# Kernel tuning notes

Hardware: AMD Instinct MI355X
Metric: run time of the kernel (lower is better)

## Reference

```python
import jax, jax.numpy as jnp
import numpy as np

B, T, E = 4, 1024, 1024
H, MULT = 16, 2
HD = E // H
SCALE = HD ** -0.5


def setup_inputs() -> dict:
    key = jax.random.key(0)
    ks = jax.random.split(key, 9)
    s = 0.02
    return {
        "hidden_states": jax.random.normal(ks[0], (B, T, E), jnp.float32),
        "attention_mask": jnp.zeros((B, 1, T, T), jnp.float32),
        "Wq": jax.random.normal(ks[1], (E, E), jnp.float32) * s,
        "bq": jnp.zeros((E,), jnp.float32),
        "Wk": jax.random.normal(ks[2], (MULT * E, E), jnp.float32) * s,
        "bk": jnp.zeros((MULT * E,), jnp.float32),
        "Wv": jax.random.normal(ks[3], (MULT * E, E), jnp.float32) * s,
        "bv": jnp.zeros((MULT * E,), jnp.float32),
        "Wo": jax.random.normal(ks[4], (E, E), jnp.float32) * s,
        "bo": jnp.zeros((E,), jnp.float32),
    }


def reference(hidden_states, attention_mask, Wq, bq, Wk, bk, Wv, bv, Wo, bo):
    x = hidden_states  # [B, T, E]
    # q projection, scaled
    q = (jnp.einsum("bte,fe->btf", x, Wq) + bq) * SCALE  # [B,T,E]
    q = q.reshape(B, T, H, HD).transpose(0, 2, 1, 3)      # [B,H,T,HD]
    # k/v project to multiplier-expanded dim, then _shape with seq_len=-1:
    # [B,T,MULT*E] -> view(B, T*MULT, H, HD) (torch view semantics) -> [B,H,T*MULT,HD]
    k = jnp.einsum("bte,fe->btf", x, Wk) + bk             # [B,T,MULT*E]
    k = k.reshape(B, T * MULT, H, HD).transpose(0, 2, 1, 3)
    v = jnp.einsum("bte,fe->btf", x, Wv) + bv
    v = v.reshape(B, T * MULT, H, HD).transpose(0, 2, 1, 3)

    S = T * MULT  # src_len; src_len0 = T
    attn = jnp.einsum("bhtd,bhsd->bhts", q, k)            # [B,H,T,S]
    # custom mask broadcast: view src as [MULT, src_len0] and add mask[:, :, :, None, :]
    attn = attn.reshape(B, H, T, MULT, T) + attention_mask[:, :, :, None, :]
    attn = attn.reshape(B, H, T, S)
    attn = jax.nn.softmax(attn, axis=-1)
    out = jnp.einsum("bhts,bhsd->bhtd", attn, v)          # [B,H,T,HD]
    out = out.transpose(0, 2, 1, 3).reshape(B, T, E)
    out = jnp.einsum("bte,fe->btf", out, Wo) + bo
    return out
```

## Files before the change

kernel.cpp:

```cpp
#include <hip/hip_runtime.h>
#include <math.h>

#define BB    4
#define TT    1024
#define EE    1024
#define HH    16
#define HDIM  64
#define SS    2048
#define MROWS 4096
#define QSCALE 0.18033688011112f
#define LOG2E  1.4426950408889634f

typedef short  s8v  __attribute__((ext_vector_type(8)));
typedef float  f4v  __attribute__((ext_vector_type(4)));

__device__ __forceinline__ unsigned short f2bf(float f) {
    union { float f; unsigned u; } c; c.f = f;
    unsigned u = c.u + 0x7FFFu + ((c.u >> 16) & 1u);
    return (unsigned short)(u >> 16);
}
__device__ __forceinline__ float bflo(unsigned u) {
    union { unsigned u; float f; } c; c.u = u << 16; return c.f;
}
__device__ __forceinline__ float bfhi(unsigned u) {
    union { unsigned u; float f; } c; c.u = u & 0xffff0000u; return c.f;
}

__device__ __forceinline__ void async16(const void* g, void* l) {
    __builtin_amdgcn_global_load_lds(
        (const __attribute__((address_space(1))) unsigned int*)g,
        (__attribute__((address_space(3))) unsigned int*)l,
        16, 0, 0);
}

__global__ __launch_bounds__(256) void cvt6_kernel(
    const float* __restrict__ x,  const float* __restrict__ wq,
    const float* __restrict__ wk, const float* __restrict__ wv,
    const float* __restrict__ wo, const float* __restrict__ mk,
    unsigned short* __restrict__ xb,  unsigned short* __restrict__ wqb,
    unsigned short* __restrict__ wkb, unsigned short* __restrict__ wvb,
    unsigned short* __restrict__ wob, unsigned short* __restrict__ mbb)
{
    const int total = 3670016;
    int i = blockIdx.x * 256 + threadIdx.x;
    const int stride = gridDim.x * 256;
    for (; i < total; i += stride) {
        const float* s; unsigned short* d; int off; float sc = 1.0f;
        if (i < 1048576)      { s = x;  d = xb;  off = i; }
        else if (i < 1310720) { s = wq; d = wqb; off = i - 1048576; }
        else if (i < 1835008) { s = wk; d = wkb; off = i - 1310720; }
        else if (i < 2359296) { s = wv; d = wvb; off = i - 1835008; }
        else if (i < 2621440) { s = wo; d = wob; off = i - 2359296; }
        else                  { s = mk; d = mbb; off = i - 2621440; sc = LOG2E; }
        float4 v = ((const float4*)s)[off];
        ushort4 o;
        o.x = f2bf(v.x * sc); o.y = f2bf(v.y * sc);
        o.z = f2bf(v.z * sc); o.w = f2bf(v.w * sc);
        ((ushort4*)d)[off] = o;
    }
}

#define GEMM_KLOOP(Aptr, Wptr, Ksz)                                            \
    for (int k0 = 0; k0 < (Ksz); k0 += 32) {                                   \
        _Pragma("unroll")                                                      \
        for (int it = 0; it < 2; ++it) {                                       \
            int f = (it * 4 + w) * 64 + lane;                                  \
            int r = f >> 2, g = (f & 3) * 8;                                   \
            async16((Aptr) + (size_t)(m0 + r) * (Ksz) + k0 + g,                \
                    As + (it * 4 + w) * 512);                                  \
            async16((Wptr) + (size_t)(n0 + r) * (Ksz) + k0 + g,                \
                    Bs + (it * 4 + w) * 512);                                  \
        }                                                                      \
        __syncthreads();                                                       \
        s8v af[4], bf[4];                                                      \
        _Pragma("unroll")                                                      \
        for (int i = 0; i < 4; ++i)                                            \
            af[i] = *(const s8v*)(As + (wm + i * 16 + col16) * 32 + quad * 8); \
        _Pragma("unroll")                                                      \
        for (int j = 0; j < 4; ++j)                                            \
            bf[j] = *(const s8v*)(Bs + (wn + j * 16 + col16) * 32 + quad * 8); \
        _Pragma("unroll")                                                      \
        for (int i = 0; i < 4; ++i)                                            \
            _Pragma("unroll")                                                  \
            for (int j = 0; j < 4; ++j)                                        \
                acc[i][j] = __builtin_amdgcn_mfma_f32_16x16x32_bf16(           \
                    af[i], bf[j], acc[i][j], 0, 0, 0);                         \
        __syncthreads();                                                       \
    }

__global__ __launch_bounds__(256, 3) void gemm_qk_kernel(
    const unsigned short* __restrict__ X,  const unsigned short* __restrict__ Wq,
    const unsigned short* __restrict__ Wk, const float* __restrict__ bq,
    const float* __restrict__ bk, unsigned short* __restrict__ qp,
    unsigned short* __restrict__ kp)
{
    __shared__ __align__(16) unsigned short As[128 * 32];
    __shared__ __align__(16) unsigned short Bs[128 * 32];

    const int tid = threadIdx.x;
    const int lane = tid & 63, w = tid >> 6;
    const int wm = (w & 1) * 64, wn = (w >> 1) * 64;
    const int col16 = lane & 15, quad = lane >> 4;
    const int m0 = blockIdx.x * 128;
    const bool isQ = blockIdx.y < 8;
    const int n0 = blockIdx.y * 128;
    const unsigned short* Wrow = isQ ? Wq + (size_t)n0 * EE
                                     : Wk + (size_t)(n0 - EE) * EE;

    f4v acc[4][4];
#pragma unroll
    for (int i = 0; i < 4; ++i)
#pragma unroll
        for (int j = 0; j < 4; ++j) acc[i][j] = (f4v)0.0f;

    for (int k0 = 0; k0 < EE; k0 += 32) {
#pragma unroll
        for (int it = 0; it < 2; ++it) {
            int f = (it * 4 + w) * 64 + lane;
            int r = f >> 2, g = (f & 3) * 8;
            async16(X + (size_t)(m0 + r) * EE + k0 + g, As + (it * 4 + w) * 512);
            async16(Wrow + (size_t)r * EE + k0 + g, Bs + (it * 4 + w) * 512);
        }
        __syncthreads();
        s8v af[4], bf[4];
#pragma unroll
        for (int i = 0; i < 4; ++i)
            af[i] = *(const s8v*)(As + (wm + i * 16 + col16) * 32 + quad * 8);
#pragma unroll
        for (int j = 0; j < 4; ++j)
            bf[j] = *(const s8v*)(Bs + (wn + j * 16 + col16) * 32 + quad * 8);
#pragma unroll
        for (int i = 0; i < 4; ++i)
#pragma unroll
            for (int j = 0; j < 4; ++j)
                acc[i][j] = __builtin_amdgcn_mfma_f32_16x16x32_bf16(
                    af[i], bf[j], acc[i][j], 0, 0, 0);
        __syncthreads();
    }

#pragma unroll
    for (int j = 0; j < 4; ++j) {
        const int n = n0 + wn + j * 16 + col16;
        const float bn = isQ ? bq[n] : bk[n - EE];
#pragma unroll
        for (int i = 0; i < 4; ++i) {
            const int mb = m0 + wm + i * 16 + quad * 4;
#pragma unroll
            for (int r = 0; r < 4; ++r) {
                const int m = mb + r;
                float c = acc[i][j][r] + bn;
                if (isQ) {
                    qp[(size_t)m * EE + n] = f2bf(c * QSCALE);
                } else {
                    const int nk = n - EE;
                    const int mm = nk >> 10, h = (nk >> 6) & 15, d = nk & 63;
                    const int b_ = m >> 10, t = m & 1023;
                    const int s = 2 * t + mm;
                    kp[((size_t)(b_ * HH + h) * SS + s) * HDIM + d] = f2bf(c);
                }
            }
        }
    }
}

template <int LAYOUT, int OUTF32, int Ksz, int Nsz>
__global__ __launch_bounds__(256, 3) void gemm_mfma_kernel(
    const unsigned short* __restrict__ A, const unsigned short* __restrict__ W,
    const float* __restrict__ bias, void* __restrict__ Cout, float alpha)
{
    __shared__ __align__(16) unsigned short As[128 * 32];
    __shared__ __align__(16) unsigned short Bs[128 * 32];

    const int tid = threadIdx.x;
    const int lane = tid & 63, w = tid >> 6;
    const int wm = (w & 1) * 64, wn = (w >> 1) * 64;
    const int col16 = lane & 15, quad = lane >> 4;
    const int m0 = blockIdx.x * 128;
    const int n0 = blockIdx.y * 128;

    f4v acc[4][4];
#pragma unroll
    for (int i = 0; i < 4; ++i)
#pragma unroll
        for (int j = 0; j < 4; ++j) acc[i][j] = (f4v)0.0f;

    GEMM_KLOOP(A, W, Ksz)

#pragma unroll
    for (int j = 0; j < 4; ++j) {
        const int n = n0 + wn + j * 16 + col16;
        const float bn = (LAYOUT == 2) ? 0.0f : bias[n];
#pragma unroll
        for (int i = 0; i < 4; ++i) {
            const int mb = m0 + wm + i * 16 + quad * 4;
#pragma unroll
            for (int r = 0; r < 4; ++r) {
                const int m = mb + r;
                float c = (acc[i][j][r] + ((LAYOUT == 2) ? bias[m] : bn)) * alpha;
                if (LAYOUT == 0) {
                    if (OUTF32) ((float*)Cout)[(size_t)m * Nsz + n] = c;
                    else ((unsigned short*)Cout)[(size_t)m * Nsz + n] = f2bf(c);
                } else {
                    const int mm = m >> 10, h = (m >> 6) & 15, d = m & 63;
                    const int b_ = n >> 10, t = n & 1023;
                    const int s = 2 * t + mm;
                    ((unsigned short*)Cout)[((size_t)(b_ * HH + h) * HDIM + d) * SS + s] = f2bf(c);
                }
            }
        }
    }
}

__global__ __launch_bounds__(256, 4) void attn_mfma3_kernel(
    const unsigned short* __restrict__ Q, const unsigned short* __restrict__ Kh,
    const unsigned short* __restrict__ Vt, const unsigned short* __restrict__ Mb,
    unsigned short* __restrict__ O)
{
    constexpr int PT = 68;
    __shared__ __align__(16) unsigned short K0[64 * PT];
    __shared__ __align__(16) unsigned short K1[64 * PT];
    __shared__ __align__(16) unsigned short V0[64 * PT];
    __shared__ __align__(16) unsigned short V1[64 * PT];

    const int tid = threadIdx.x;
    const int lane = tid & 63, w = tid >> 6;
    const int col16 = lane & 15, quad = lane >> 4;

    const int gid = blockIdx.x;
    const int v = gid & 7, j = gid >> 3;
    const int bh = v * 8 + (j >> 4);
    const int t0 = (j & 15) * 64;
    const int b_ = bh >> 4, h = bh & 15;

    const unsigned short* Qrow =
        Q + (size_t)(b_ * TT + t0 + w * 16 + col16) * EE + h * HDIM;
    const s8v qf0 = *(const s8v*)(Qrow + quad * 8);
    const s8v qf1 = *(const s8v*)(Qrow + 32 + quad * 8);

    f4v oacc[4];
#pragma unroll
    for (int jd = 0; jd < 4; ++jd) oacc[jd] = (f4v)0.0f;
    float mrun = -INFINITY;
    f4v l4 = (f4v)0.0f;

    const unsigned short* Kb   = Kh + (size_t)bh * SS * HDIM;
    const unsigned short* Vb   = Vt + (size_t)bh * HDIM * SS;
    const unsigned short* Mrow = Mb + (size_t)b_ * TT * TT
                               + (size_t)(t0 + w * 16 + col16) * TT;
    const int myrow = (w * 16 + col16) * PT;

    for (int it16 = 0; it16 < 16; ++it16) {
        const int t2b = it16 * 64;

        uint2 mm[4];
#pragma unroll
        for (int js = 0; js < 4; ++js)
            mm[js] = *(const uint2*)(Mrow + t2b + js * 16 + quad * 4);

        __syncthreads();
#pragma unroll
        for (int st = 0; st < 2; ++st) {
            int idx = tid + st * 256;
            int r = idx >> 3, c = (idx & 7) * 8;
            *(uint4*)(K0 + r * PT + c) = *(const uint4*)(Kb + (size_t)(t2b + r) * HDIM + c);
            *(uint4*)(K1 + r * PT + c) = *(const uint4*)(Kb + (size_t)(1024 + t2b + r) * HDIM + c);
            *(uint4*)(V0 + r * PT + c) = *(const uint4*)(Vb + (size_t)r * SS + t2b + c);
            *(uint4*)(V1 + r * PT + c) = *(const uint4*)(Vb + (size_t)r * SS + 1024 + t2b + c);
        }
        __syncthreads();

        f4v s0acc[4], s1acc[4];
#pragma unroll
        for (int js = 0; js < 4; ++js) {
            f4v mv;
            mv[0] = bflo(mm[js].x); mv[1] = bfhi(mm[js].x);
            mv[2] = bflo(mm[js].y); mv[3] = bfhi(mm[js].y);
            s0acc[js] = mv; s1acc[js] = mv;
        }
#pragma unroll
        for (int ks = 0; ks < 2; ++ks) {
            const s8v bq_ = ks ? qf1 : qf0;
#pragma unroll
            for (int js = 0; js < 4; ++js) {
                s8v ak0 = *(const s8v*)(K0 + (js * 16 + col16) * PT + ks * 32 + quad * 8);
                s8v ak1 = *(const s8v*)(K1 + (js * 16 + col16) * PT + ks * 32 + quad * 8);
                s0acc[js] = __builtin_amdgcn_mfma_f32_16x16x32_bf16(ak0, bq_, s0acc[js], 0, 0, 0);
                s1acc[js] = __builtin_amdgcn_mfma_f32_16x16x32_bf16(ak1, bq_, s1acc[js], 0, 0, 0);
            }
        }

        float tm0 = fmaxf(fmaxf(s0acc[0][0], s0acc[0][1]), fmaxf(s0acc[0][2], s0acc[0][3]));
        float tm1 = fmaxf(fmaxf(s0acc[1][0], s0acc[1][1]), fmaxf(s0acc[1][2], s0acc[1][3]));
        float tm2 = fmaxf(fmaxf(s0acc[2][0], s0acc[2][1]), fmaxf(s0acc[2][2], s0acc[2][3]));
        float tm3 = fmaxf(fmaxf(s0acc[3][0], s0acc[3][1]), fmaxf(s0acc[3][2], s0acc[3][3]));
        float tn0 = fmaxf(fmaxf(s1acc[0][0], s1acc[0][1]), fmaxf(s1acc[0][2], s1acc[0][3]));
        float tn1 = fmaxf(fmaxf(s1acc[1][0], s1acc[1][1]), fmaxf(s1acc[1][2], s1acc[1][3]));
        float tn2 = fmaxf(fmaxf(s1acc[2][0], s1acc[2][1]), fmaxf(s1acc[2][2], s1acc[2][3]));
        float tn3 = fmaxf(fmaxf(s1acc[3][0], s1acc[3][1]), fmaxf(s1acc[3][2], s1acc[3][3]));
        float tmax = fmaxf(fmaxf(fmaxf(tm0, tm1), fmaxf(tm2, tm3)),
                           fmaxf(fmaxf(tn0, tn1), fmaxf(tn2, tn3)));

        if (!__all(tmax - mrun <= 10.0f)) {
            float tfull = fmaxf(tmax, __shfl_xor(tmax, 16));
            tfull = fmaxf(tfull, __shfl_xor(tfull, 32));
            const float mnew = fmaxf(mrun, tfull);
            const float scl = __builtin_amdgcn_exp2f(mrun - mnew);
            l4 *= scl;
            float sclr[4];
#pragma unroll
            for (int r = 0; r < 4; ++r) sclr[r] = __shfl(scl, quad * 4 + r);
#pragma unroll
            for (int jd = 0; jd < 4; ++jd)
#pragma unroll
                for (int r = 0; r < 4; ++r) oacc[jd][r] *= sclr[r];
            mrun = mnew;
        }

        unsigned pk0[8], pk1[8];
#pragma unroll
        for (int js = 0; js < 4; ++js) {
            f4v p0 = s0acc[js] - mrun;
            f4v p1 = s1acc[js] - mrun;
#pragma unroll
            for (int r = 0; r < 4; ++r) {
                p0[r] = __builtin_amdgcn_exp2f(p0[r]);
                p1[r] = __builtin_amdgcn_exp2f(p1[r]);
            }
            l4 += p0 + p1;
            __asm__("v_cvt_pk_bf16_f32 %0, %1, %2" : "=v"(pk0[js*2])   : "v"(p0[0]), "v"(p0[1]));
            __asm__("v_cvt_pk_bf16_f32 %0, %1, %2" : "=v"(pk0[js*2+1]) : "v"(p0[2]), "v"(p0[3]));
            __asm__("v_cvt_pk_bf16_f32 %0, %1, %2" : "=v"(pk1[js*2])   : "v"(p1[0]), "v"(p1[1]));
            __asm__("v_cvt_pk_bf16_f32 %0, %1, %2" : "=v"(pk1[js*2+1]) : "v"(p1[2]), "v"(p1[3]));
        }

        __syncthreads();

#pragma unroll
        for (int js = 0; js < 4; ++js) {
            *(uint2*)(K0 + myrow + js * 16 + quad * 4) = make_uint2(pk0[js*2], pk0[js*2+1]);
            *(uint2*)(K1 + myrow + js * 16 + quad * 4) = make_uint2(pk1[js*2], pk1[js*2+1]);
        }
        __syncthreads();

#pragma unroll
        for (int ks = 0; ks < 2; ++ks) {
            s8v p0 = *(const s8v*)(K0 + myrow + ks * 32 + quad * 8);
            s8v p1 = *(const s8v*)(K1 + myrow + ks * 32 + quad * 8);
#pragma unroll
            for (int jd = 0; jd < 4; ++jd) {
                s8v v0_ = *(const s8v*)(V0 + (jd * 16 + col16) * PT + ks * 32 + quad * 8);
                s8v v1_ = *(const s8v*)(V1 + (jd * 16 + col16) * PT + ks * 32 + quad * 8);
                oacc[jd] = __builtin_amdgcn_mfma_f32_16x16x32_bf16(p0, v0_, oacc[jd], 0, 0, 0);
                oacc[jd] = __builtin_amdgcn_mfma_f32_16x16x32_bf16(p1, v1_, oacc[jd], 0, 0, 0);
            }
        }
    }

    float lr = l4[0] + l4[1] + l4[2] + l4[3];
    lr += __shfl_xor(lr, 16);
    lr += __shfl_xor(lr, 32);
    const float inv = 1.0f / lr;
    float invr[4];
#pragma unroll
    for (int r = 0; r < 4; ++r) invr[r] = __shfl(inv, quad * 4 + r);
#pragma unroll
    for (int r = 0; r < 4; ++r) {
        const int t = t0 + w * 16 + quad * 4 + r;
#pragma unroll
        for (int jd = 0; jd < 4; ++jd)
            O[(size_t)(b_ * TT + t) * EE + h * HDIM + jd * 16 + col16] =
                f2bf(oacc[jd][r] * invr[r]);
    }
}

extern "C" void kernel_launch(void* const* d_in, const int* in_sizes, int n_in,
                              void* d_out, int out_size, void* d_ws, size_t ws_size,
                              hipStream_t stream)
{
    (void)in_sizes; (void)n_in; (void)out_size; (void)ws_size;

    const float* x    = (const float*)d_in[0];
    const float* mask = (const float*)d_in[1];
    const float* Wq   = (const float*)d_in[2];
    const float* bq   = (const float*)d_in[3];
    const float* Wk   = (const float*)d_in[4];
    const float* bk   = (const float*)d_in[5];
    const float* Wv   = (const float*)d_in[6];
    const float* bv   = (const float*)d_in[7];
    const float* Wo   = (const float*)d_in[8];
    const float* bo   = (const float*)d_in[9];
    float* out = (float*)d_out;

    unsigned short* xb  = (unsigned short*)d_ws;
    unsigned short* wqb = xb  + (size_t)MROWS * EE;
    unsigned short* wkb = wqb + (size_t)EE * EE;
    unsigned short* wvb = wkb + (size_t)2 * EE * EE;
    unsigned short* wob = wvb + (size_t)2 * EE * EE;
    unsigned short* mb  = wob + (size_t)EE * EE;
    unsigned short* qp  = mb  + (size_t)BB * TT * TT;
    unsigned short* kp  = qp  + (size_t)MROWS * EE;
    unsigned short* vt  = kp  + (size_t)BB * HH * SS * HDIM;
    unsigned short* ao  = vt  + (size_t)BB * HH * SS * HDIM;

    dim3 blk(256);

    cvt6_kernel<<<4096, blk, 0, stream>>>(x, Wq, Wk, Wv, Wo, mask,
                                          xb, wqb, wkb, wvb, wob, mb);
    gemm_qk_kernel<<<dim3(32, 24), blk, 0, stream>>>(xb, wqb, wkb, bq, bk, qp, kp);
    gemm_mfma_kernel<2, 0, EE, MROWS><<<dim3(16, 32), blk, 0, stream>>>(
        wvb, xb, bv, vt, 1.0f);
    attn_mfma3_kernel<<<dim3(1024), blk, 0, stream>>>(qp, kp, vt, mb, ao);
    gemm_mfma_kernel<0, 1, EE, EE><<<dim3(32, 8), blk, 0, stream>>>(
        ao, wob, bo, out, 1.0f);
}
```

Baseline: 268.2 us.

## Prefetch next K/V/mask tile into registers during attention compute

Result: slower. 370.9 us (+38.3%).

```diff
diff --git a/kernel.cpp b/kernel.cpp
--- a/kernel.cpp
+++ b/kernel.cpp
@@ -211,7 +211,7 @@
     }
 }
 
-__global__ __launch_bounds__(256, 4) void attn_mfma3_kernel(
+__global__ __launch_bounds__(256, 4) void attn_mfma4_kernel(
     const unsigned short* __restrict__ Q, const unsigned short* __restrict__ Kh,
     const unsigned short* __restrict__ Vt, const unsigned short* __restrict__ Mb,
     unsigned short* __restrict__ O)
@@ -248,35 +248,57 @@
     const unsigned short* Mrow = Mb + (size_t)b_ * TT * TT
                                + (size_t)(t0 + w * 16 + col16) * TT;
     const int myrow = (w * 16 + col16) * PT;
+    const int r0 = tid >> 3, c0 = (tid & 7) * 8;
+
+    uint4 kv[8];
+    uint2 mmc[4];
+
+#define PREF_KV(T2B)                                                           \
+    kv[0] = *(const uint4*)(Kb + (size_t)((T2B) + r0) * HDIM + c0);            \
+    kv[1] = *(const uint4*)(Kb + (size_t)((T2B) + r0 + 32) * HDIM + c0);       \
+    kv[2] = *(const uint4*)(Kb + (size_t)(1024 + (T2B) + r0) * HDIM + c0);     \
+    kv[3] = *(const uint4*)(Kb + (size_t)(1024 + (T2B) + r0 + 32) * HDIM + c0);\
+    kv[4] = *(const uint4*)(Vb + (size_t)r0 * SS + (T2B) + c0);                \
+    kv[5] = *(const uint4*)(Vb + (size_t)(r0 + 32) * SS + (T2B) + c0);         \
+    kv[6] = *(const uint4*)(Vb + (size_t)r0 * SS + 1024 + (T2B) + c0);         \
+    kv[7] = *(const uint4*)(Vb + (size_t)(r0 + 32) * SS + 1024 + (T2B) + c0);
+
+    PREF_KV(0)
+#pragma unroll
+    for (int js = 0; js < 4; ++js)
+        mmc[js] = *(const uint2*)(Mrow + js * 16 + quad * 4);
 
     for (int it16 = 0; it16 < 16; ++it16) {
-        const int t2b = it16 * 64;
-
-        uint2 mm[4];
-#pragma unroll
-        for (int js = 0; js < 4; ++js)
-            mm[js] = *(const uint2*)(Mrow + t2b + js * 16 + quad * 4);
-
         __syncthreads();
-#pragma unroll
-        for (int st = 0; st < 2; ++st) {
-            int idx = tid + st * 256;
-            int r = idx >> 3, c = (idx & 7) * 8;
-            *(uint4*)(K0 + r * PT + c) = *(const uint4*)(Kb + (size_t)(t2b + r) * HDIM + c);
-            *(uint4*)(K1 + r * PT + c) = *(const uint4*)(Kb + (size_t)(1024 + t2b + r) * HDIM + c);
-            *(uint4*)(V0 + r * PT + c) = *(const uint4*)(Vb + (size_t)r * SS + t2b + c);
-            *(uint4*)(V1 + r * PT + c) = *(const uint4*)(Vb + (size_t)r * SS + 1024 + t2b + c);
-        }
+
+        *(uint4*)(K0 + r0 * PT + c0)        = kv[0];
+        *(uint4*)(K0 + (r0 + 32) * PT + c0) = kv[1];
+        *(uint4*)(K1 + r0 * PT + c0)        = kv[2];
+        *(uint4*)(K1 + (r0 + 32) * PT + c0) = kv[3];
+        *(uint4*)(V0 + r0 * PT + c0)        = kv[4];
+        *(uint4*)(V0 + (r0 + 32) * PT + c0) = kv[5];
+        *(uint4*)(V1 + r0 * PT + c0)        = kv[6];
+        *(uint4*)(V1 + (r0 + 32) * PT + c0) = kv[7];
         __syncthreads();
 
         f4v s0acc[4], s1acc[4];
 #pragma unroll
         for (int js = 0; js < 4; ++js) {
             f4v mv;
-            mv[0] = bflo(mm[js].x); mv[1] = bfhi(mm[js].x);
-            mv[2] = bflo(mm[js].y); mv[3] = bfhi(mm[js].y);
+            mv[0] = bflo(mmc[js].x); mv[1] = bfhi(mmc[js].x);
+            mv[2] = bflo(mmc[js].y); mv[3] = bfhi(mmc[js].y);
             s0acc[js] = mv; s1acc[js] = mv;
         }
+
+        {
+            const int t2n = ((it16 + 1) & 15) * 64;
+            PREF_KV(t2n)
+#pragma unroll
+            for (int js = 0; js < 4; ++js)
+                mmc[js] = *(const uint2*)(Mrow + t2n + js * 16 + quad * 4);
+        }
+
+        __builtin_amdgcn_s_setprio(1);
 #pragma unroll
         for (int ks = 0; ks < 2; ++ks) {
             const s8v bq_ = ks ? qf1 : qf0;
@@ -288,6 +310,7 @@
                 s1acc[js] = __builtin_amdgcn_mfma_f32_16x16x32_bf16(ak1, bq_, s1acc[js], 0, 0, 0);
             }
         }
+        __builtin_amdgcn_s_setprio(0);
 
         float tm0 = fmaxf(fmaxf(s0acc[0][0], s0acc[0][1]), fmaxf(s0acc[0][2], s0acc[0][3]));
         float tm1 = fmaxf(fmaxf(s0acc[1][0], s0acc[1][1]), fmaxf(s0acc[1][2], s0acc[1][3]));
@@ -340,8 +363,8 @@
             *(uint2*)(K0 + myrow + js * 16 + quad * 4) = make_uint2(pk0[js*2], pk0[js*2+1]);
             *(uint2*)(K1 + myrow + js * 16 + quad * 4) = make_uint2(pk1[js*2], pk1[js*2+1]);
         }
-        __syncthreads();
-
+
+        __builtin_amdgcn_s_setprio(1);
 #pragma unroll
         for (int ks = 0; ks < 2; ++ks) {
             s8v p0 = *(const s8v*)(K0 + myrow + ks * 32 + quad * 8);
@@ -354,7 +377,9 @@
                 oacc[jd] = __builtin_amdgcn_mfma_f32_16x16x32_bf16(p1, v1_, oacc[jd], 0, 0, 0);
             }
         }
-    }
+        __builtin_amdgcn_s_setprio(0);
+    }
+#undef PREF_KV
 
     float lr = l4[0] + l4[1] + l4[2] + l4[3];
     lr += __shfl_xor(lr, 16);
@@ -409,7 +434,7 @@
     gemm_qk_kernel<<<dim3(32, 24), blk, 0, stream>>>(xb, wqb, wkb, bq, bk, qp, kp);
     gemm_mfma_kernel<2, 0, EE, MROWS><<<dim3(16, 32), blk, 0, stream>>>(
         wvb, xb, bv, vt, 1.0f);
-    attn_mfma3_kernel<<<dim3(1024), blk, 0, stream>>>(qp, kp, vt, mb, ao);
+    attn_mfma4_kernel<<<dim3(1024), blk, 0, stream>>>(qp, kp, vt, mb, ao);
     gemm_mfma_kernel<0, 1, EE, EE><<<dim3(32, 8), blk, 0, stream>>>(
         ao, wob, bo, out, 1.0f);
 }
```

## Prefetch next K/V/mask tiles into registers and drop a redundant barrier

Applied to the files above, without the earlier changes.

Result: faster. 258.5 us (-3.6%).

```diff
diff --git a/kernel.cpp b/kernel.cpp
--- a/kernel.cpp
+++ b/kernel.cpp
@@ -211,7 +211,7 @@
     }
 }
 
-__global__ __launch_bounds__(256, 4) void attn_mfma3_kernel(
+__global__ __launch_bounds__(256, 4) void attn_mfma5_kernel(
     const unsigned short* __restrict__ Q, const unsigned short* __restrict__ Kh,
     const unsigned short* __restrict__ Vt, const unsigned short* __restrict__ Mb,
     unsigned short* __restrict__ O)
@@ -248,35 +248,68 @@
     const unsigned short* Mrow = Mb + (size_t)b_ * TT * TT
                                + (size_t)(t0 + w * 16 + col16) * TT;
     const int myrow = (w * 16 + col16) * PT;
+    const int r0 = tid >> 3, c0 = (tid & 7) * 8;
+
+    uint4 kA0, kA1, kB0, kB1;
+    uint4 vA0, vA1, vB0, vB1;
+    uint2 mA0, mA1, mA2, mA3;
+
+#define PREF_K(T2B)                                                            \
+    kA0 = *(const uint4*)(Kb + (size_t)((T2B) + r0) * HDIM + c0);              \
+    kA1 = *(const uint4*)(Kb + (size_t)((T2B) + r0 + 32) * HDIM + c0);         \
+    kB0 = *(const uint4*)(Kb + (size_t)(1024 + (T2B) + r0) * HDIM + c0);       \
+    kB1 = *(const uint4*)(Kb + (size_t)(1024 + (T2B) + r0 + 32) * HDIM + c0);
+#define PREF_V(T2B)                                                            \
+    vA0 = *(const uint4*)(Vb + (size_t)r0 * SS + (T2B) + c0);                  \
+    vA1 = *(const uint4*)(Vb + (size_t)(r0 + 32) * SS + (T2B) + c0);           \
+    vB0 = *(const uint4*)(Vb + (size_t)r0 * SS + 1024 + (T2B) + c0);           \
+    vB1 = *(const uint4*)(Vb + (size_t)(r0 + 32) * SS + 1024 + (T2B) + c0);
+#define PREF_M(T2B)                                                            \
+    mA0 = *(const uint2*)(Mrow + (T2B) + 0 * 16 + quad * 4);                   \
+    mA1 = *(const uint2*)(Mrow + (T2B) + 1 * 16 + quad * 4);                   \
+    mA2 = *(const uint2*)(Mrow + (T2B) + 2 * 16 + quad * 4);                   \
+    mA3 = *(const uint2*)(Mrow + (T2B) + 3 * 16 + quad * 4);
+
+    PREF_K(0)
+    PREF_V(0)
+    PREF_M(0)
 
     for (int it16 = 0; it16 < 16; ++it16) {
-        const int t2b = it16 * 64;
-
-        uint2 mm[4];
-#pragma unroll
-        for (int js = 0; js < 4; ++js)
-            mm[js] = *(const uint2*)(Mrow + t2b + js * 16 + quad * 4);
-
         __syncthreads();
-#pragma unroll
-        for (int st = 0; st < 2; ++st) {
-            int idx = tid + st * 256;
-            int r = idx >> 3, c = (idx & 7) * 8;
-            *(uint4*)(K0 + r * PT + c) = *(const uint4*)(Kb + (size_t)(t2b + r) * HDIM + c);
-            *(uint4*)(K1 + r * PT + c) = *(const uint4*)(Kb + (size_t)(1024 + t2b + r) * HDIM + c);
-            *(uint4*)(V0 + r * PT + c) = *(const uint4*)(Vb + (size_t)r * SS + t2b + c);
-            *(uint4*)(V1 + r * PT + c) = *(const uint4*)(Vb + (size_t)r * SS + 1024 + t2b + c);
-        }
+
+        *(uint4*)(K0 + r0 * PT + c0)        = kA0;
+        *(uint4*)(K0 + (r0 + 32) * PT + c0) = kA1;
+        *(uint4*)(K1 + r0 * PT + c0)        = kB0;
+        *(uint4*)(K1 + (r0 + 32) * PT + c0) = kB1;
+        *(uint4*)(V0 + r0 * PT + c0)        = vA0;
+        *(uint4*)(V0 + (r0 + 32) * PT + c0) = vA1;
+        *(uint4*)(V1 + r0 * PT + c0)        = vB0;
+        *(uint4*)(V1 + (r0 + 32) * PT + c0) = vB1;
+
+        f4v s0acc[4], s1acc[4];
+        {
+            f4v mv;
+            mv[0] = bflo(mA0.x); mv[1] = bfhi(mA0.x);
+            mv[2] = bflo(mA0.y); mv[3] = bfhi(mA0.y);
+            s0acc[0] = mv; s1acc[0] = mv;
+            mv[0] = bflo(mA1.x); mv[1] = bfhi(mA1.x);
+            mv[2] = bflo(mA1.y); mv[3] = bfhi(mA1.y);
+            s0acc[1] = mv; s1acc[1] = mv;
+            mv[0] = bflo(mA2.x); mv[1] = bfhi(mA2.x);
+            mv[2] = bflo(mA2.y); mv[3] = bfhi(mA2.y);
+            s0acc[2] = mv; s1acc[2] = mv;
+            mv[0] = bflo(mA3.x); mv[1] = bfhi(mA3.x);
+            mv[2] = bflo(mA3.y); mv[3] = bfhi(mA3.y);
+            s0acc[3] = mv; s1acc[3] = mv;
+        }
+
+        const int t2n = ((it16 + 1) & 15) * 64;
+        PREF_K(t2n)
+        PREF_M(t2n)
+
         __syncthreads();
 
-        f4v s0acc[4], s1acc[4];
-#pragma unroll
-        for (int js = 0; js < 4; ++js) {
-            f4v mv;
-            mv[0] = bflo(mm[js].x); mv[1] = bfhi(mm[js].x);
-            mv[2] = bflo(mm[js].y); mv[3] = bfhi(mm[js].y);
-            s0acc[js] = mv; s1acc[js] = mv;
-        }
+        __builtin_amdgcn_s_setprio(1);
 #pragma unroll
         for (int ks = 0; ks < 2; ++ks) {
             const s8v bq_ = ks ? qf1 : qf0;
@@ -288,6 +321,7 @@
                 s1acc[js] = __builtin_amdgcn_mfma_f32_16x16x32_bf16(ak1, bq_, s1acc[js], 0, 0, 0);
             }
         }
+        __builtin_amdgcn_s_setprio(0);
 
         float tm0 = fmaxf(fmaxf(s0acc[0][0], s0acc[0][1]), fmaxf(s0acc[0][2], s0acc[0][3]));
         float tm1 = fmaxf(fmaxf(s0acc[1][0], s0acc[1][1]), fmaxf(s0acc[1][2], s0acc[1][3]));
@@ -333,6 +367,8 @@
             __asm__("v_cvt_pk_bf16_f32 %0, %1, %2" : "=v"(pk1[js*2+1]) : "v"(p1[2]), "v"(p1[3]));
         }
 
+        PREF_V(t2n)
+
         __syncthreads();
 
 #pragma unroll
@@ -340,8 +376,8 @@
             *(uint2*)(K0 + myrow + js * 16 + quad * 4) = make_uint2(pk0[js*2], pk0[js*2+1]);
             *(uint2*)(K1 + myrow + js * 16 + quad * 4) = make_uint2(pk1[js*2], pk1[js*2+1]);
         }
-        __syncthreads();
-
+
+        __builtin_amdgcn_s_setprio(1);
 #pragma unroll
         for (int ks = 0; ks < 2; ++ks) {
             s8v p0 = *(const s8v*)(K0 + myrow + ks * 32 + quad * 8);
@@ -354,7 +390,11 @@
                 oacc[jd] = __builtin_amdgcn_mfma_f32_16x16x32_bf16(p1, v1_, oacc[jd], 0, 0, 0);
             }
         }
-    }
+        __builtin_amdgcn_s_setprio(0);
+    }
+#undef PREF_K
+#undef PREF_V
+#undef PREF_M
 
     float lr = l4[0] + l4[1] + l4[2] + l4[3];
     lr += __shfl_xor(lr, 16);
@@ -409,7 +449,7 @@
     gemm_qk_kernel<<<dim3(32, 24), blk, 0, stream>>>(xb, wqb, wkb, bq, bk, qp, kp);
     gemm_mfma_kernel<2, 0, EE, MROWS><<<dim3(16, 32), blk, 0, stream>>>(
         wvb, xb, bv, vt, 1.0f);
-    attn_mfma3_kernel<<<dim3(1024), blk, 0, stream>>>(qp, kp, vt, mb, ao);
+    attn_mfma5_kernel<<<dim3(1024), blk, 0, stream>>>(qp, kp, vt, mb, ao);
     gemm_mfma_kernel<0, 1, EE, EE><<<dim3(32, 8), blk, 0, stream>>>(
         ao, wob, bo, out, 1.0f);
 }
```

## Restructure attention kernel: 2 waves × 32 rows, register prefetch, separate P buffer

Applied to the files above, without the earlier changes.

Result: slower. 279.8 us (+4.3%).

```diff
diff --git a/kernel.cpp b/kernel.cpp
--- a/kernel.cpp
+++ b/kernel.cpp
@@ -211,19 +211,19 @@
     }
 }
 
-__global__ __launch_bounds__(256, 4) void attn_mfma3_kernel(
+__global__ __launch_bounds__(128, 2) void attn_mfma9_kernel(
     const unsigned short* __restrict__ Q, const unsigned short* __restrict__ Kh,
     const unsigned short* __restrict__ Vt, const unsigned short* __restrict__ Mb,
     unsigned short* __restrict__ O)
 {
     constexpr int PT = 68;
-    __shared__ __align__(16) unsigned short K0[64 * PT];
-    __shared__ __align__(16) unsigned short K1[64 * PT];
-    __shared__ __align__(16) unsigned short V0[64 * PT];
-    __shared__ __align__(16) unsigned short V1[64 * PT];
+    __shared__ __align__(16) unsigned short Ks[64 * PT];
+    __shared__ __align__(16) unsigned short Vs[64 * PT];
+    __shared__ __align__(16) unsigned short Ps[64 * PT];
 
     const int tid = threadIdx.x;
-    const int lane = tid & 63, w = tid >> 6;
+    const int w = tid >> 6;
+    const int lane = tid & 63;
     const int col16 = lane & 15, quad = lane >> 4;
 
     const int gid = blockIdx.x;
@@ -232,145 +232,218 @@
     const int t0 = (j & 15) * 64;
     const int b_ = bh >> 4, h = bh & 15;
 
-    const unsigned short* Qrow =
-        Q + (size_t)(b_ * TT + t0 + w * 16 + col16) * EE + h * HDIM;
-    const s8v qf0 = *(const s8v*)(Qrow + quad * 8);
-    const s8v qf1 = *(const s8v*)(Qrow + 32 + quad * 8);
-
-    f4v oacc[4];
-#pragma unroll
-    for (int jd = 0; jd < 4; ++jd) oacc[jd] = (f4v)0.0f;
-    float mrun = -INFINITY;
-    f4v l4 = (f4v)0.0f;
+    const unsigned short* Qr0 =
+        Q + (size_t)(b_ * TT + t0 + w * 32 + col16) * EE + h * HDIM;
+    const unsigned short* Qr1 = Qr0 + 16 * EE;
+    const s8v qf00 = *(const s8v*)(Qr0 + quad * 8);
+    const s8v qf01 = *(const s8v*)(Qr0 + 32 + quad * 8);
+    const s8v qf10 = *(const s8v*)(Qr1 + quad * 8);
+    const s8v qf11 = *(const s8v*)(Qr1 + 32 + quad * 8);
+
+    f4v oacc[2][4];
+#pragma unroll
+    for (int tn = 0; tn < 2; ++tn)
+#pragma unroll
+        for (int jd = 0; jd < 4; ++jd) oacc[tn][jd] = (f4v)0.0f;
+    float mrun0 = -INFINITY, mrun1 = -INFINITY;
+    f4v l40 = (f4v)0.0f, l41 = (f4v)0.0f;
 
     const unsigned short* Kb   = Kh + (size_t)bh * SS * HDIM;
     const unsigned short* Vb   = Vt + (size_t)bh * HDIM * SS;
-    const unsigned short* Mrow = Mb + (size_t)b_ * TT * TT
-                               + (size_t)(t0 + w * 16 + col16) * TT;
-    const int myrow = (w * 16 + col16) * PT;
-
-    for (int it16 = 0; it16 < 16; ++it16) {
-        const int t2b = it16 * 64;
-
-        uint2 mm[4];
-#pragma unroll
-        for (int js = 0; js < 4; ++js)
-            mm[js] = *(const uint2*)(Mrow + t2b + js * 16 + quad * 4);
-
+    const unsigned short* Mr0  = Mb + (size_t)b_ * TT * TT
+                               + (size_t)(t0 + w * 32 + col16) * TT;
+    const unsigned short* Mr1  = Mr0 + (size_t)16 * TT;
+    const int myrow0 = (w * 32 + col16) * PT;
+    const int myrow1 = myrow0 + 16 * PT;
+    const int sr0 = tid >> 3, sc0 = (tid & 7) * 8;
+
+    uint4 kS0, kS1, kS2, kS3;
+    uint4 vS0, vS1, vS2, vS3;
+    uint2 m00, m01, m02, m03, m10, m11, m12, m13;
+
+#define PREF_K(SB)                                                             \
+    kS0 = *(const uint4*)(Kb + (size_t)((SB) + sr0) * HDIM + sc0);             \
+    kS1 = *(const uint4*)(Kb + (size_t)((SB) + sr0 + 16) * HDIM + sc0);        \
+    kS2 = *(const uint4*)(Kb + (size_t)((SB) + sr0 + 32) * HDIM + sc0);        \
+    kS3 = *(const uint4*)(Kb + (size_t)((SB) + sr0 + 48) * HDIM + sc0);
+#define PREF_V(SB)                                                             \
+    vS0 = *(const uint4*)(Vb + (size_t)sr0 * SS + (SB) + sc0);                 \
+    vS1 = *(const uint4*)(Vb + (size_t)(sr0 + 16) * SS + (SB) + sc0);          \
+    vS2 = *(const uint4*)(Vb + (size_t)(sr0 + 32) * SS + (SB) + sc0);          \
+    vS3 = *(const uint4*)(Vb + (size_t)(sr0 + 48) * SS + (SB) + sc0);
+#define PREF_M(T2)                                                             \
+    m00 = *(const uint2*)(Mr0 + (T2) + 0 * 16 + quad * 4);                     \
+    m01 = *(const uint2*)(Mr0 + (T2) + 1 * 16 + quad * 4);                     \
+    m02 = *(const uint2*)(Mr0 + (T2) + 2 * 16 + quad * 4);                     \
+    m03 = *(const uint2*)(Mr0 + (T2) + 3 * 16 + quad * 4);                     \
+    m10 = *(const uint2*)(Mr1 + (T2) + 0 * 16 + quad * 4);                     \
+    m11 = *(const uint2*)(Mr1 + (T2) + 1 * 16 + quad * 4);                     \
+    m12 = *(const uint2*)(Mr1 + (T2) + 2 * 16 + quad * 4);                     \
+    m13 = *(const uint2*)(Mr1 + (T2) + 3 * 16 + quad * 4);
+
+    PREF_K(0)
+    PREF_V(0)
+    PREF_M(0)
+
+    for (int it = 0; it < 32; ++it) {
         __syncthreads();
-#pragma unroll
-        for (int st = 0; st < 2; ++st) {
-            int idx = tid + st * 256;
-            int r = idx >> 3, c = (idx & 7) * 8;
-            *(uint4*)(K0 + r * PT + c) = *(const uint4*)(Kb + (size_t)(t2b + r) * HDIM + c);
-            *(uint4*)(K1 + r * PT + c) = *(const uint4*)(Kb + (size_t)(1024 + t2b + r) * HDIM + c);
-            *(uint4*)(V0 + r * PT + c) = *(const uint4*)(Vb + (size_t)r * SS + t2b + c);
-            *(uint4*)(V1 + r * PT + c) = *(const uint4*)(Vb + (size_t)r * SS + 1024 + t2b + c);
-        }
+
+        *(uint4*)(Ks + sr0 * PT + sc0)        = kS0;
+        *(uint4*)(Ks + (sr0 + 16) * PT + sc0) = kS1;
+        *(uint4*)(Ks + (sr0 + 32) * PT + sc0) = kS2;
+        *(uint4*)(Ks + (sr0 + 48) * PT + sc0) = kS3;
+        *(uint4*)(Vs + sr0 * PT + sc0)        = vS0;
+        *(uint4*)(Vs + (sr0 + 16) * PT + sc0) = vS1;
+        *(uint4*)(Vs + (sr0 + 32) * PT + sc0) = vS2;
+        *(uint4*)(Vs + (sr0 + 48) * PT + sc0) = vS3;
+
+        f4v sacc[2][4];
+        {
+            f4v mv;
+            mv[0] = bflo(m00.x); mv[1] = bfhi(m00.x);
+            mv[2] = bflo(m00.y); mv[3] = bfhi(m00.y); sacc[0][0] = mv;
+            mv[0] = bflo(m01.x); mv[1] = bfhi(m01.x);
+            mv[2] = bflo(m01.y); mv[3] = bfhi(m01.y); sacc[0][1] = mv;
+            mv[0] = bflo(m02.x); mv[1] = bfhi(m02.x);
+            mv[2] = bflo(m02.y); mv[3] = bfhi(m02.y); sacc[0][2] = mv;
+            mv[0] = bflo(m03.x); mv[1] = bfhi(m03.x);
+            mv[2] = bflo(m03.y); mv[3] = bfhi(m03.y); sacc[0][3] = mv;
+            mv[0] = bflo(m10.x); mv[1] = bfhi(m10.x);
+            mv[2] = bflo(m10.y); mv[3] = bfhi(m10.y); sacc[1][0] = mv;
+            mv[0] = bflo(m11.x); mv[1] = bfhi(m11.x);
+            mv[2] = bflo(m11.y); mv[3] = bfhi(m11.y); sacc[1][1] = mv;
+            mv[0] = bflo(m12.x); mv[1] = bfhi(m12.x);
+            mv[2] = bflo(m12.y); mv[3] = bfhi(m12.y); sacc[1][2] = mv;
+            mv[0] = bflo(m13.x); mv[1] = bfhi(m13.x);
+            mv[2] = bflo(m13.y); mv[3] = bfhi(m13.y); sacc[1][3] = mv;
+        }
+
+        {
+            const int itn = (it + 1) & 31;
+            const int sbn = ((itn >> 4) << 10) + ((itn & 15) << 6);
+            const int t2n = (itn & 15) << 6;
+            PREF_K(sbn)
+            PREF_V(sbn)
+            PREF_M(t2n)
+        }
+
         __syncthreads();
 
-        f4v s0acc[4], s1acc[4];
+        __builtin_amdgcn_s_setprio(1);
+#pragma unroll
+        for (int ks = 0; ks < 2; ++ks) {
+            const s8v bq0 = ks ? qf01 : qf00;
+            const s8v bq1 = ks ? qf11 : qf10;
+#pragma unroll
+            for (int js = 0; js < 4; ++js) {
+                s8v ak = *(const s8v*)(Ks + (js * 16 + col16) * PT + ks * 32 + quad * 8);
+                sacc[0][js] = __builtin_amdgcn_mfma_f32_16x16x32_bf16(ak, bq0, sacc[0][js], 0, 0, 0);
+                sacc[1][js] = __builtin_amdgcn_mfma_f32_16x16x32_bf16(ak, bq1, sacc[1][js], 0, 0, 0);
+            }
+        }
+        __builtin_amdgcn_s_setprio(0);
+
+        float ta0 = fmaxf(fmaxf(sacc[0][0][0], sacc[0][0][1]), fmaxf(sacc[0][0][2], sacc[0][0][3]));
+        float ta1 = fmaxf(fmaxf(sacc[0][1][0], sacc[0][1][1]), fmaxf(sacc[0][1][2], sacc[0][1][3]));
+        float ta2 = fmaxf(fmaxf(sacc[0][2][0], sacc[0][2][1]), fmaxf(sacc[0][2][2], sacc[0][2][3]));
+        float ta3 = fmaxf(fmaxf(sacc[0][3][0], sacc[0][3][1]), fmaxf(sacc[0][3][2], sacc[0][3][3]));
+        float tb0 = fmaxf(fmaxf(sacc[1][0][0], sacc[1][0][1]), fmaxf(sacc[1][0][2], sacc[1][0][3]));
+        float tb1 = fmaxf(fmaxf(sacc[1][1][0], sacc[1][1][1]), fmaxf(sacc[1][1][2], sacc[1][1][3]));
+        float tb2 = fmaxf(fmaxf(sacc[1][2][0], sacc[1][2][1]), fmaxf(sacc[1][2][2], sacc[1][2][3]));
+        float tb3 = fmaxf(fmaxf(sacc[1][3][0], sacc[1][3][1]), fmaxf(sacc[1][3][2], sacc[1][3][3]));
+        float tmax0 = fmaxf(fmaxf(ta0, ta1), fmaxf(ta2, ta3));
+        float tmax1 = fmaxf(fmaxf(tb0, tb1), fmaxf(tb2, tb3));
+
+        if (!__all(tmax0 - mrun0 <= 10.0f && tmax1 - mrun1 <= 10.0f)) {
+            float tf0 = fmaxf(tmax0, __shfl_xor(tmax0, 16));
+            tf0 = fmaxf(tf0, __shfl_xor(tf0, 32));
+            float tf1 = fmaxf(tmax1, __shfl_xor(tmax1, 16));
+            tf1 = fmaxf(tf1, __shfl_xor(tf1, 32));
+            const float mn0 = fmaxf(mrun0, tf0);
+            const float mn1 = fmaxf(mrun1, tf1);
+            const float sc0_ = __builtin_amdgcn_exp2f(mrun0 - mn0);
+            const float sc1_ = __builtin_amdgcn_exp2f(mrun1 - mn1);
+            l40 *= sc0_; l41 *= sc1_;
+            float sr[2][4];
+#pragma unroll
+            for (int r = 0; r < 4; ++r) {
+                sr[0][r] = __shfl(sc0_, quad * 4 + r);
+                sr[1][r] = __shfl(sc1_, quad * 4 + r);
+            }
+#pragma unroll
+            for (int jd = 0; jd < 4; ++jd)
+#pragma unroll
+                for (int r = 0; r < 4; ++r) {
+                    oacc[0][jd][r] *= sr[0][r];
+                    oacc[1][jd][r] *= sr[1][r];
+                }
+            mrun0 = mn0; mrun1 = mn1;
+        }
+
+        unsigned pk0[8], pk1[8];
 #pragma unroll
         for (int js = 0; js < 4; ++js) {
-            f4v mv;
-            mv[0] = bflo(mm[js].x); mv[1] = bfhi(mm[js].x);
-            mv[2] = bflo(mm[js].y); mv[3] = bfhi(mm[js].y);
-            s0acc[js] = mv; s1acc[js] = mv;
-        }
-#pragma unroll
-        for (int ks = 0; ks < 2; ++ks) {
-            const s8v bq_ = ks ? qf1 : qf0;
-#pragma unroll
-            for (int js = 0; js < 4; ++js) {
-                s8v ak0 = *(const s8v*)(K0 + (js * 16 + col16) * PT + ks * 32 + quad * 8);
-                s8v ak1 = *(const s8v*)(K1 + (js * 16 + col16) * PT + ks * 32 + quad * 8);
-                s0acc[js] = __builtin_amdgcn_mfma_f32_16x16x32_bf16(ak0, bq_, s0acc[js], 0, 0, 0);
-                s1acc[js] = __builtin_amdgcn_mfma_f32_16x16x32_bf16(ak1, bq_, s1acc[js], 0, 0, 0);
-            }
-        }
-
-        float tm0 = fmaxf(fmaxf(s0acc[0][0], s0acc[0][1]), fmaxf(s0acc[0][2], s0acc[0][3]));
-        float tm1 = fmaxf(fmaxf(s0acc[1][0], s0acc[1][1]), fmaxf(s0acc[1][2], s0acc[1][3]));
-        float tm2 = fmaxf(fmaxf(s0acc[2][0], s0acc[2][1]), fmaxf(s0acc[2][2], s0acc[2][3]));
-        float tm3 = fmaxf(fmaxf(s0acc[3][0], s0acc[3][1]), fmaxf(s0acc[3][2], s0acc[3][3]));
-        float tn0 = fmaxf(fmaxf(s1acc[0][0], s1acc[0][1]), fmaxf(s1acc[0][2], s1acc[0][3]));
-        float tn1 = fmaxf(fmaxf(s1acc[1][0], s1acc[1][1]), fmaxf(s1acc[1][2], s1acc[1][3]));
-        float tn2 = fmaxf(fmaxf(s1acc[2][0], s1acc[2][1]), fmaxf(s1acc[2][2], s1acc[2][3]));
-        float tn3 = fmaxf(fmaxf(s1acc[3][0], s1acc[3][1]), fmaxf(s1acc[3][2], s1acc[3][3]));
-        float tmax = fmaxf(fmaxf(fmaxf(tm0, tm1), fmaxf(tm2, tm3)),
-                           fmaxf(fmaxf(tn0, tn1), fmaxf(tn2, tn3)));
-
-        if (!__all(tmax - mrun <= 10.0f)) {
-            float tfull = fmaxf(tmax, __shfl_xor(tmax, 16));
-            tfull = fmaxf(tfull, __shfl_xor(tfull, 32));
-            const float mnew = fmaxf(mrun, tfull);
-            const float scl = __builtin_amdgcn_exp2f(mrun - mnew);
-            l4 *= scl;
-            float sclr[4];
-#pragma unroll
-            for (int r = 0; r < 4; ++r) sclr[r] = __shfl(scl, quad * 4 + r);
-#pragma unroll
-            for (int jd = 0; jd < 4; ++jd)
-#pragma unroll
-                for (int r = 0; r < 4; ++r) oacc[jd][r] *= sclr[r];
-            mrun = mnew;
-        }
-
-        unsigned pk0[8], pk1[8];
-#pragma unroll
-        for (int js = 0; js < 4; ++js) {
-            f4v p0 = s0acc[js] - mrun;
-            f4v p1 = s1acc[js] - mrun;
+            f4v p0 = sacc[0][js] - mrun0;
+            f4v p1 = sacc[1][js] - mrun1;
 #pragma unroll
             for (int r = 0; r < 4; ++r) {
                 p0[r] = __builtin_amdgcn_exp2f(p0[r]);
                 p1[r] = __builtin_amdgcn_exp2f(p1[r]);
             }
-            l4 += p0 + p1;
+            l40 += p0; l41 += p1;
             __asm__("v_cvt_pk_bf16_f32 %0, %1, %2" : "=v"(pk0[js*2])   : "v"(p0[0]), "v"(p0[1]));
             __asm__("v_cvt_pk_bf16_f32 %0, %1, %2" : "=v"(pk0[js*2+1]) : "v"(p0[2]), "v"(p0[3]));
             __asm__("v_cvt_pk_bf16_f32 %0, %1, %2" : "=v"(pk1[js*2])   : "v"(p1[0]), "v"(p1[1]));
             __asm__("v_cvt_pk_bf16_f32 %0, %1, %2" : "=v"(pk1[js*2+1]) : "v"(p1[2]), "v"(p1[3]));
         }
 
-        __syncthreads();
-
 #pragma unroll
         for (int js = 0; js < 4; ++js) {
-            *(uint2*)(K0 + myrow + js * 16 + quad * 4) = make_uint2(pk0[js*2], pk0[js*2+1]);
-            *(uint2*)(K1 + myrow + js * 16 + quad * 4) = make_uint2(pk1[js*2], pk1[js*2+1]);
-        }
-        __syncthreads();
-
+            *(uint2*)(Ps + myrow0 + js * 16 + quad * 4) = make_uint2(pk0[js*2], pk0[js*2+1]);
+            *(uint2*)(Ps + myrow1 + js * 16 + quad * 4) = make_uint2(pk1[js*2], pk1[js*2+1]);
+        }
+
+        __builtin_amdgcn_s_setprio(1);
 #pragma unroll
         for (int ks = 0; ks < 2; ++ks) {
-            s8v p0 = *(const s8v*)(K0 + myrow + ks * 32 + quad * 8);
-            s8v p1 = *(const s8v*)(K1 + myrow + ks * 32 + quad * 8);
+            s8v pa0 = *(const s8v*)(Ps + myrow0 + ks * 32 + quad * 8);
+            s8v pa1 = *(const s8v*)(Ps + myrow1 + ks * 32 + quad * 8);
 #pragma unroll
             for (int jd = 0; jd < 4; ++jd) {
-                s8v v0_ = *(const s8v*)(V0 + (jd * 16 + col16) * PT + ks * 32 + quad * 8);
-                s8v v1_ = *(const s8v*)(V1 + (jd * 16 + col16) * PT + ks * 32 + quad * 8);
-                oacc[jd] = __builtin_amdgcn_mfma_f32_16x16x32_bf16(p0, v0_, oacc[jd], 0, 0, 0);
-                oacc[jd] = __builtin_amdgcn_mfma_f32_16x16x32_bf16(p1, v1_, oacc[jd], 0, 0, 0);
-            }
-        }
-    }
-
-    float lr = l4[0] + l4[1] + l4[2] + l4[3];
-    lr += __shfl_xor(lr, 16);
-    lr += __shfl_xor(lr, 32);
-    const float inv = 1.0f / lr;
-    float invr[4];
-#pragma unroll
-    for (int r = 0; r < 4; ++r) invr[r] = __shfl(inv, quad * 4 + r);
+                s8v vf = *(const s8v*)(Vs + (jd * 16 + col16) * PT + ks * 32 + quad * 8);
+                oacc[0][jd] = __builtin_amdgcn_mfma_f32_16x16x32_bf16(pa0, vf, oacc[0][jd], 0, 0, 0);
+                oacc[1][jd] = __builtin_amdgcn_mfma_f32_16x16x32_bf16(pa1, vf, oacc[1][jd], 0, 0, 0);
+            }
+        }
+        __builtin_amdgcn_s_setprio(0);
+    }
+#undef PREF_K
+#undef PREF_V
+#undef PREF_M
+
+    float lr0 = l40[0] + l40[1] + l40[2] + l40[3];
+    lr0 += __shfl_xor(lr0, 16);
+    lr0 += __shfl_xor(lr0, 32);
+    float lr1 = l41[0] + l41[1] + l41[2] + l41[3];
+    lr1 += __shfl_xor(lr1, 16);
+    lr1 += __shfl_xor(lr1, 32);
+    const float inv0 = 1.0f / lr0, inv1 = 1.0f / lr1;
+    float ivr[2][4];
 #pragma unroll
     for (int r = 0; r < 4; ++r) {
-        const int t = t0 + w * 16 + quad * 4 + r;
-#pragma unroll
-        for (int jd = 0; jd < 4; ++jd)
-            O[(size_t)(b_ * TT + t) * EE + h * HDIM + jd * 16 + col16] =
-                f2bf(oacc[jd][r] * invr[r]);
-    }
+        ivr[0][r] = __shfl(inv0, quad * 4 + r);
+        ivr[1][r] = __shfl(inv1, quad * 4 + r);
+    }
+#pragma unroll
+    for (int tn = 0; tn < 2; ++tn)
+#pragma unroll
+        for (int r = 0; r < 4; ++r) {
+            const int t = t0 + w * 32 + tn * 16 + quad * 4 + r;
+#pragma unroll
+            for (int jd = 0; jd < 4; ++jd)
+                O[(size_t)(b_ * TT + t) * EE + h * HDIM + jd * 16 + col16] =
+                    f2bf(oacc[tn][jd][r] * ivr[tn][r]);
+        }
 }
 
 extern "C" void kernel_launch(void* const* d_in, const int* in_sizes, int n_in,
@@ -409,7 +482,7 @@
     gemm_qk_kernel<<<dim3(32, 24), blk, 0, stream>>>(xb, wqb, wkb, bq, bk, qp, kp);
     gemm_mfma_kernel<2, 0, EE, MROWS><<<dim3(16, 32), blk, 0, stream>>>(
         wvb, xb, bv, vt, 1.0f);
-    attn_mfma3_kernel<<<dim3(1024), blk, 0, stream>>>(qp, kp, vt, mb, ao);
+    attn_mfma9_kernel<<<dim3(1024), dim3(128), 0, stream>>>(qp, kp, vt, mb, ao);
     gemm_mfma_kernel<0, 1, EE, EE><<<dim3(32, 8), blk, 0, stream>>>(
         ao, wob, bo, out, 1.0f);
 }
```
